# Kernel optimization log

Measured on AMD Instinct MI355X. Metric: run time of the kernel, lower is better.

Reference implementation:

```python
import jax, jax.numpy as jnp
import numpy as np

B, S, E, H, V, T, L = 64, 512, 512, 512, 32000, 2, 1


def setup_inputs() -> dict:
    key = jax.random.key(0)
    ks = jax.random.split(key, 12)
    # xavier_normal std for h0/c0 of shape (L, B, H): fan_in=B*H, fan_out=L*H
    xav = float(np.sqrt(2.0 / (B * H + L * H)))
    s = 1.0 / float(np.sqrt(H))  # pytorch LSTM default uniform bound
    return {
        "sentence": jax.random.randint(ks[0], (B, S), 0, V, dtype=jnp.int64),
        "h0": jax.random.normal(ks[1], (L, B, H), jnp.float32) * xav,
        "c0": jax.random.normal(ks[2], (L, B, H), jnp.float32) * xav,
        "emb": jax.random.normal(ks[3], (V, E), jnp.float32),
        "W_ih": jax.random.uniform(ks[4], (4 * H, E), jnp.float32, -s, s),
        "W_hh": jax.random.uniform(ks[5], (4 * H, H), jnp.float32, -s, s),
        "b_ih": jax.random.uniform(ks[6], (4 * H,), jnp.float32, -s, s),
        "b_hh": jax.random.uniform(ks[7], (4 * H,), jnp.float32, -s, s),
        "W_lin": jax.random.uniform(ks[8], (T, H), jnp.float32, -s, s),
        "b_lin": jax.random.uniform(ks[9], (T,), jnp.float32, -s, s),
    }


def reference(sentence, h0, c0, emb, W_ih, W_hh, b_ih, b_hh, W_lin, b_lin):
    x = emb[sentence]                                   # [B,S,E]
    # precompute input-to-gate projections for all timesteps
    xg = jnp.einsum("bse,ge->bsg", x, W_ih) + (b_ih + b_hh)  # [B,S,4H]

    def step(carry, xt):
        h, c = carry                                    # [B,H] each
        g = xt + h @ W_hh.T                             # [B,4H]
        i, f, gc, o = jnp.split(g, 4, axis=-1)          # torch gate order i,f,g,o
        i = jax.nn.sigmoid(i)
        f = jax.nn.sigmoid(f)
        gc = jnp.tanh(gc)
        o = jax.nn.sigmoid(o)
        c = f * c + i * gc
        h = o * jnp.tanh(c)
        return (h, c), h

    (hn, cn), hs = jax.lax.scan(step, (h0[0], c0[0]), xg.transpose(1, 0, 2))
    lstm_out = hs.transpose(1, 0, 2)                    # [B,S,H]
    # dropout is identity at inference; torch code indexes drop[-1,:,:] =
    # LAST BATCH SAMPLE (batch_first=True quirk) -> [S,H]
    last = lstm_out[-1]                                 # [S,H]
    return last @ W_lin.T + b_lin                       # [S,T]
```

## Files before the change

### kernel.cpp

```cpp
#include <hip/hip_runtime.h>
#include <hip/hip_bf16.h>


#define NB 64

#define HIDX(e) ((((e) >> 4) * 20) + ((e) & 15))

__global__ __launch_bounds__(256) void xg_gemm_k(
    const int* __restrict__ sent, const float* __restrict__ emb,
    const float* __restrict__ W_ih, const float* __restrict__ b_ih,
    const float* __restrict__ b_hh, float* __restrict__ xg)
{
    __shared__ float As[16][65];
    __shared__ float Bs[16][65];
    __shared__ int aidx[64];
    const int tid = threadIdx.x;
    const int t0 = blockIdx.x * 64;
    const int n0 = blockIdx.y * 64;
    if (tid < 64) aidx[tid] = sent[63 * 512 + t0 + tid];
    __syncthreads();

    const int kk = tid & 15;
    const int mm = tid >> 4;
    const int tx = tid & 15, ty = tid >> 4;
    float acc[4][4] = {};

    for (int kb = 0; kb < 512; kb += 16) {
        #pragma unroll
        for (int j = 0; j < 4; j++) {
            int m = mm + j * 16;
            As[kk][m] = emb[(size_t)aidx[m] * 512 + kb + kk];
            Bs[kk][m] = W_ih[(size_t)(n0 + m) * 512 + kb + kk];
        }
        __syncthreads();
        #pragma unroll
        for (int k = 0; k < 16; k++) {
            float a[4], bv[4];
            #pragma unroll
            for (int i = 0; i < 4; i++) a[i] = As[k][ty * 4 + i];
            #pragma unroll
            for (int j = 0; j < 4; j++) bv[j] = Bs[k][tx * 4 + j];
            #pragma unroll
            for (int i = 0; i < 4; i++)
                #pragma unroll
                for (int j = 0; j < 4; j++)
                    acc[i][j] += a[i] * bv[j];
        }
        __syncthreads();
    }

    #pragma unroll
    for (int i = 0; i < 4; i++) {
        int t = t0 + ty * 4 + i;
        #pragma unroll
        for (int j = 0; j < 4; j++) {
            int col = n0 + tx * 4 + j;
            xg[(size_t)t * 2048 + col] = acc[i][j] + b_ih[col] + b_hh[col];
        }
    }
}

__global__ __launch_bounds__(256, 1) void lstm_seq_k(
    const float* __restrict__ h0, const float* __restrict__ c0,
    const float* __restrict__ W_hh, const float* __restrict__ xg,
    float* __restrict__ hs,
    unsigned long long* __restrict__ sA,
    unsigned long long* __restrict__ sB)
{
    __shared__ float hbuf[32 * 20];
    __shared__ float gacc[32];
    __shared__ float cbuf[8];

    const int tid = threadIdx.x;
    const int b = blockIdx.x;
    const int cg = tid & 31;
    const int rg = tid >> 5;

    int grow[4];
    #pragma unroll
    for (int r = 0; r < 4; r++) {
        int rl = rg * 4 + r;
        grow[r] = (rl >> 3) * 512 + b * 8 + (rl & 7);
    }

    float4 wv[4][4];
    #pragma unroll
    for (int r = 0; r < 4; r++)
        #pragma unroll
        for (int cq = 0; cq < 4; cq++)
            wv[r][cq] = *(const float4*)&W_hh[(size_t)grow[r] * 512 + cg * 16 + cq * 4];

    if (tid < 8) cbuf[tid] = c0[63 * 512 + b * 8 + tid];
    __syncthreads();

    for (int t = 0; t < 512; t++) {
        float xgp[4];
        if (cg == 0) {
            #pragma unroll
            for (int r = 0; r < 4; r++)
                xgp[r] = xg[(size_t)t * 2048 + grow[r]];
        }

        if (t == 0) {
            hbuf[HIDX(tid)]       = h0[63 * 512 + tid];
            hbuf[HIDX(tid + 256)] = h0[63 * 512 + tid + 256];
        } else {
            unsigned long long* src = ((t - 1) & 1) ? sB : sA;
            unsigned long long* p0 = &src[tid];
            unsigned long long* p1 = &src[tid + 256];
            const unsigned int expt = (unsigned int)t;
            unsigned long long v0, v1;
            for (;;) {
                v0 = __hip_atomic_load(p0, __ATOMIC_RELAXED, __HIP_MEMORY_SCOPE_AGENT);
                v1 = __hip_atomic_load(p1, __ATOMIC_RELAXED, __HIP_MEMORY_SCOPE_AGENT);
                if ((unsigned int)(v0 >> 32) == expt &&
                    (unsigned int)(v1 >> 32) == expt) break;
            }
            hbuf[HIDX(tid)]       = __uint_as_float((unsigned int)v0);
            hbuf[HIDX(tid + 256)] = __uint_as_float((unsigned int)v1);
        }
        __syncthreads();

        float4 hv[4];
        #pragma unroll
        for (int cq = 0; cq < 4; cq++)
            hv[cq] = *(const float4*)&hbuf[cg * 20 + cq * 4];

        float acc[4];
        #pragma unroll
        for (int r = 0; r < 4; r++) {
            float s = 0.f;
            #pragma unroll
            for (int cq = 0; cq < 4; cq++) {
                s += wv[r][cq].x * hv[cq].x;
                s += wv[r][cq].y * hv[cq].y;
                s += wv[r][cq].z * hv[cq].z;
                s += wv[r][cq].w * hv[cq].w;
            }
            acc[r] = s;
        }

        #pragma unroll
        for (int r = 0; r < 4; r++) {
            #pragma unroll
            for (int m = 16; m >= 1; m >>= 1)
                acc[r] += __shfl_xor(acc[r], m, 64);
        }
        if (cg == 0) {
            #pragma unroll
            for (int r = 0; r < 4; r++)
                gacc[rg * 4 + r] = acc[r] + xgp[r];
        }
        __syncthreads();

        if (tid < 8) {
            float gi = gacc[tid];
            float gf = gacc[8 + tid];
            float gc = gacc[16 + tid];
            float go = gacc[24 + tid];
            float ii = 1.f / (1.f + __expf(-gi));
            float ff = 1.f / (1.f + __expf(-gf));
            float cc = 1.f - 2.f / (__expf(2.f * gc) + 1.f);
            float oo = 1.f / (1.f + __expf(-go));
            float cn = ff * cbuf[tid] + ii * cc;
            cbuf[tid] = cn;
            float th = 1.f - 2.f / (__expf(2.f * cn) + 1.f);
            float hval = oo * th;

            hs[(size_t)t * 512 + b * 8 + tid] = hval;

            unsigned long long* dst = (t & 1) ? sB : sA;
            unsigned long long pv =
                ((unsigned long long)(unsigned int)(t + 1) << 32) |
                (unsigned long long)__float_as_uint(hval);
            __hip_atomic_store(&dst[b * 8 + tid], pv,
                               __ATOMIC_RELAXED, __HIP_MEMORY_SCOPE_AGENT);
        }
    }
}

__global__ __launch_bounds__(256) void final_linear_k(
    const float* __restrict__ hs, const float* __restrict__ W_lin,
    const float* __restrict__ b_lin, float* __restrict__ out)
{
    const int tid = threadIdx.x;
    const int wave = tid >> 6;
    const int lane = tid & 63;
    const int s = blockIdx.x * 4 + wave;
    const float* h = hs + (size_t)s * 512;
    float a0 = 0.f, a1 = 0.f;
    #pragma unroll
    for (int k0 = 0; k0 < 512; k0 += 64) {
        float hv = h[k0 + lane];
        a0 += hv * W_lin[k0 + lane];
        a1 += hv * W_lin[512 + k0 + lane];
    }
    #pragma unroll
    for (int m = 32; m >= 1; m >>= 1) {
        a0 += __shfl_xor(a0, m, 64);
        a1 += __shfl_xor(a1, m, 64);
    }
    if (lane == 0) {
        out[s * 2]     = a0 + b_lin[0];
        out[s * 2 + 1] = a1 + b_lin[1];
    }
}

extern "C" void kernel_launch(void* const* d_in, const int* in_sizes, int n_in,
                              void* d_out, int out_size, void* d_ws, size_t ws_size,
                              hipStream_t stream)
{
    const int*   sent  = (const int*)d_in[0];
    const float* h0    = (const float*)d_in[1];
    const float* c0    = (const float*)d_in[2];
    const float* emb   = (const float*)d_in[3];
    const float* W_ih  = (const float*)d_in[4];
    const float* W_hh  = (const float*)d_in[5];
    const float* b_ih  = (const float*)d_in[6];
    const float* b_hh  = (const float*)d_in[7];
    const float* W_lin = (const float*)d_in[8];
    const float* b_lin = (const float*)d_in[9];
    float* out = (float*)d_out;

    char* ws = (char*)d_ws;
    float* xg = (float*)ws;
    float* hs = (float*)(ws + 4 * 1024 * 1024);
    unsigned long long* sA = (unsigned long long*)(ws + 5 * 1024 * 1024);
    unsigned long long* sB = (unsigned long long*)(ws + 5 * 1024 * 1024 + 4096);

    hipMemsetAsync(sA, 0, 2 * 4096, stream);

    dim3 g1(8, 32);
    xg_gemm_k<<<g1, 256, 0, stream>>>(sent, emb, W_ih, b_ih, b_hh, xg);
    lstm_seq_k<<<NB, 256, 0, stream>>>(h0, c0, W_hh, xg, hs, sA, sB);
    final_linear_k<<<128, 256, 0, stream>>>(hs, W_lin, b_lin, out);
}
```

Baseline: 1.005 ms.

## Assign all four gates of one hidden unit per wave, drop second barrier

```diff
diff --git a/kernel.cpp b/kernel.cpp
--- a/kernel.cpp
+++ b/kernel.cpp
@@ -1,6 +1,8 @@
 #include <hip/hip_runtime.h>
-#include <hip/hip_bf16.h>
-
+
+
+typedef float f32x4 __attribute__((ext_vector_type(4)));
+typedef unsigned long long u64;
 
 #define NB 64
 
@@ -64,12 +66,9 @@
     const float* __restrict__ h0, const float* __restrict__ c0,
     const float* __restrict__ W_hh, const float* __restrict__ xg,
     float* __restrict__ hs,
-    unsigned long long* __restrict__ sA,
-    unsigned long long* __restrict__ sB)
-{
-    __shared__ float hbuf[32 * 20];
-    __shared__ float gacc[32];
-    __shared__ float cbuf[8];
+    u64* __restrict__ sA, u64* __restrict__ sB)
+{
+    __shared__ float hb[2][648];
 
     const int tid = threadIdx.x;
     const int b = blockIdx.x;
@@ -78,102 +77,99 @@
 
     int grow[4];
     #pragma unroll
-    for (int r = 0; r < 4; r++) {
-        int rl = rg * 4 + r;
-        grow[r] = (rl >> 3) * 512 + b * 8 + (rl & 7);
-    }
-
-    float4 wv[4][4];
-    #pragma unroll
-    for (int r = 0; r < 4; r++)
-        #pragma unroll
-        for (int cq = 0; cq < 4; cq++)
-            wv[r][cq] = *(const float4*)&W_hh[(size_t)grow[r] * 512 + cg * 16 + cq * 4];
-
-    if (tid < 8) cbuf[tid] = c0[63 * 512 + b * 8 + tid];
-    __syncthreads();
-
-    for (int t = 0; t < 512; t++) {
+    for (int r = 0; r < 4; ++r)
+        grow[r] = r * 512 + b * 8 + rg;
+
+    f32x4 w[4][4];
+    #pragma unroll
+    for (int r = 0; r < 4; ++r)
+        #pragma unroll
+        for (int cq = 0; cq < 4; ++cq)
+            w[r][cq] = *(const f32x4*)&W_hh[(size_t)grow[r] * 512 + cg * 16 + cq * 4];
+
+    float creg = c0[63 * 512 + b * 8 + rg];
+
+    for (int t = 0; t < 512; ++t) {
+        #pragma unroll
+        for (int r = 0; r < 4; ++r)
+            asm volatile("" : "+v"(w[r][0]), "+v"(w[r][1]),
+                              "+v"(w[r][2]), "+v"(w[r][3]));
+
+        const int p = t & 1;
+
         float xgp[4];
         if (cg == 0) {
             #pragma unroll
-            for (int r = 0; r < 4; r++)
+            for (int r = 0; r < 4; ++r)
                 xgp[r] = xg[(size_t)t * 2048 + grow[r]];
         }
 
         if (t == 0) {
-            hbuf[HIDX(tid)]       = h0[63 * 512 + tid];
-            hbuf[HIDX(tid + 256)] = h0[63 * 512 + tid + 256];
+            hb[p][HIDX(tid)]       = h0[63 * 512 + tid];
+            hb[p][HIDX(tid + 256)] = h0[63 * 512 + tid + 256];
         } else {
-            unsigned long long* src = ((t - 1) & 1) ? sB : sA;
-            unsigned long long* p0 = &src[tid];
-            unsigned long long* p1 = &src[tid + 256];
-            const unsigned int expt = (unsigned int)t;
-            unsigned long long v0, v1;
+            u64* src = ((t - 1) & 1) ? sB : sA;
+            u64* p0 = &src[tid];
+            u64* p1 = &src[tid + 256];
+            const unsigned expt = (unsigned)t;
+            u64 v0, v1;
             for (;;) {
                 v0 = __hip_atomic_load(p0, __ATOMIC_RELAXED, __HIP_MEMORY_SCOPE_AGENT);
                 v1 = __hip_atomic_load(p1, __ATOMIC_RELAXED, __HIP_MEMORY_SCOPE_AGENT);
-                if ((unsigned int)(v0 >> 32) == expt &&
-                    (unsigned int)(v1 >> 32) == expt) break;
+                if ((unsigned)(v0 >> 32) == expt &&
+                    (unsigned)(v1 >> 32) == expt) break;
             }
-            hbuf[HIDX(tid)]       = __uint_as_float((unsigned int)v0);
-            hbuf[HIDX(tid + 256)] = __uint_as_float((unsigned int)v1);
+            hb[p][HIDX(tid)]       = __uint_as_float((unsigned)v0);
+            hb[p][HIDX(tid + 256)] = __uint_as_float((unsigned)v1);
         }
         __syncthreads();
 
-        float4 hv[4];
-        #pragma unroll
-        for (int cq = 0; cq < 4; cq++)
-            hv[cq] = *(const float4*)&hbuf[cg * 20 + cq * 4];
+        f32x4 hv[4];
+        #pragma unroll
+        for (int cq = 0; cq < 4; ++cq)
+            hv[cq] = *(const f32x4*)&hb[p][cg * 20 + cq * 4];
 
         float acc[4];
         #pragma unroll
-        for (int r = 0; r < 4; r++) {
+        for (int r = 0; r < 4; ++r) {
             float s = 0.f;
             #pragma unroll
-            for (int cq = 0; cq < 4; cq++) {
-                s += wv[r][cq].x * hv[cq].x;
-                s += wv[r][cq].y * hv[cq].y;
-                s += wv[r][cq].z * hv[cq].z;
-                s += wv[r][cq].w * hv[cq].w;
+            for (int cq = 0; cq < 4; ++cq) {
+                s += w[r][cq].x * hv[cq].x;
+                s += w[r][cq].y * hv[cq].y;
+                s += w[r][cq].z * hv[cq].z;
+                s += w[r][cq].w * hv[cq].w;
             }
             acc[r] = s;
         }
 
         #pragma unroll
-        for (int r = 0; r < 4; r++) {
+        for (int r = 0; r < 4; ++r) {
             #pragma unroll
             for (int m = 16; m >= 1; m >>= 1)
                 acc[r] += __shfl_xor(acc[r], m, 64);
         }
+
         if (cg == 0) {
-            #pragma unroll
-            for (int r = 0; r < 4; r++)
-                gacc[rg * 4 + r] = acc[r] + xgp[r];
-        }
-        __syncthreads();
-
-        if (tid < 8) {
-            float gi = gacc[tid];
-            float gf = gacc[8 + tid];
-            float gc = gacc[16 + tid];
-            float go = gacc[24 + tid];
+            float gi = acc[0] + xgp[0];
+            float gf = acc[1] + xgp[1];
+            float gc = acc[2] + xgp[2];
+            float go = acc[3] + xgp[3];
             float ii = 1.f / (1.f + __expf(-gi));
             float ff = 1.f / (1.f + __expf(-gf));
             float cc = 1.f - 2.f / (__expf(2.f * gc) + 1.f);
             float oo = 1.f / (1.f + __expf(-go));
-            float cn = ff * cbuf[tid] + ii * cc;
-            cbuf[tid] = cn;
+            float cn = ff * creg + ii * cc;
+            creg = cn;
             float th = 1.f - 2.f / (__expf(2.f * cn) + 1.f);
             float hval = oo * th;
 
-            hs[(size_t)t * 512 + b * 8 + tid] = hval;
-
-            unsigned long long* dst = (t & 1) ? sB : sA;
-            unsigned long long pv =
-                ((unsigned long long)(unsigned int)(t + 1) << 32) |
-                (unsigned long long)__float_as_uint(hval);
-            __hip_atomic_store(&dst[b * 8 + tid], pv,
+            hs[(size_t)t * 512 + b * 8 + rg] = hval;
+
+            u64* dst = (t & 1) ? sB : sA;
+            u64 pv = ((u64)(unsigned)(t + 1) << 32) |
+                     (u64)__float_as_uint(hval);
+            __hip_atomic_store(&dst[b * 8 + rg], pv,
                                __ATOMIC_RELAXED, __HIP_MEMORY_SCOPE_AGENT);
         }
     }
@@ -225,8 +221,8 @@
     char* ws = (char*)d_ws;
     float* xg = (float*)ws;
     float* hs = (float*)(ws + 4 * 1024 * 1024);
-    unsigned long long* sA = (unsigned long long*)(ws + 5 * 1024 * 1024);
-    unsigned long long* sB = (unsigned long long*)(ws + 5 * 1024 * 1024 + 4096);
+    u64* sA = (u64*)(ws + 5 * 1024 * 1024);
+    u64* sB = (u64*)(ws + 5 * 1024 * 1024 + 4096);
 
     hipMemsetAsync(sA, 0, 2 * 4096, stream);
 
```

Result: slower. 1.124 ms (+11.9%).
